# Kernel tuning notes

Measured on AMD Instinct MI355X. Metric: run time of the kernel, lower is better.

## Reference

```python
import jax, jax.numpy as jnp
import numpy as np

N = 262144  # points per batch (~4096 rays x 64 samples)
FDIM = 64   # plane feature dim
S = 512     # base plane resolution


def setup_inputs() -> dict:
    key = jax.random.key(0)
    ks = jax.random.split(key, 10)
    x = jax.random.uniform(ks[0], (N, 3), dtype=jnp.float32, minval=-1.0, maxval=1.0)
    rays_o = jnp.array([[0.0, 0.0, 1.5]], dtype=jnp.float32)  # ray origin; distances straddle 1.5/2.0
    scale = jnp.ones((3,), dtype=jnp.float32)
    plane = lambda k, s: jax.random.normal(k, (FDIM, s, s), dtype=jnp.float32)
    return {
        'x': x, 'rays_o': rays_o, 'scale': scale,
        'xy_plane': plane(ks[1], S), 'yz_plane': plane(ks[2], S), 'xz_plane': plane(ks[3], S),
        'xy_plane1': plane(ks[4], S // 2), 'yz_plane1': plane(ks[5], S // 2), 'xz_plane1': plane(ks[6], S // 2),
        'xy_plane2': plane(ks[7], S // 4), 'yz_plane2': plane(ks[8], S // 4), 'xz_plane2': plane(ks[9], S // 4),
    }


def bilinear_sample(plane, coords):
    """F.grid_sample(mode='bilinear', align_corners=True, padding_mode='zeros').
    plane: [C, H, W]; coords: [N, 2] with (x, y) in [-1, 1] (x indexes W).
    Returns [N, C]."""
    C, H, W = plane.shape
    fx = (coords[:, 0] + 1.0) * 0.5 * (W - 1)
    fy = (coords[:, 1] + 1.0) * 0.5 * (H - 1)
    x0 = jnp.floor(fx)
    y0 = jnp.floor(fy)
    wx = fx - x0
    wy = fy - y0
    x0i = x0.astype(jnp.int32)
    y0i = y0.astype(jnp.int32)

    def gather(xi, yi):
        valid = (xi >= 0) & (xi < W) & (yi >= 0) & (yi < H)
        xc = jnp.clip(xi, 0, W - 1)
        yc = jnp.clip(yi, 0, H - 1)
        v = plane[:, yc, xc]  # [C, N]
        return jnp.where(valid[None, :], v, 0.0)

    v00 = gather(x0i, y0i)
    v01 = gather(x0i + 1, y0i)
    v10 = gather(x0i, y0i + 1)
    v11 = gather(x0i + 1, y0i + 1)
    out = (v00 * (1 - wx) * (1 - wy) + v01 * wx * (1 - wy)
           + v10 * (1 - wx) * wy + v11 * wx * wy)  # [C, N]
    return out.T


def forward(x, rays_o, scale, xy0, yz0, xz0, xy1, yz1, xz1, xy2, yz2, xz2):
    xs = x * scale[None, :]
    xy_c = xs[:, :2]                                   # (x, y)
    xz_c = jnp.stack([xs[:, 0], xs[:, 2]], axis=-1)    # (x, z)
    yz_c = xs[:, 1:]                                   # (y, z)

    # laplace breakpoints: first index with distance > 1.5 / > 2.0 from rays_o[0]
    d = jnp.linalg.norm(rays_o[0][None, :] - xs, axis=-1)
    c1 = d > 1.5
    c2 = d > 2.0
    break1 = jnp.where(c1.any(), jnp.argmax(c1), 0)
    break2 = jnp.where(c2.any(), jnp.argmax(c2), 0)
    idx = jnp.arange(x.shape[0])
    # level 0: [0, break1), level 1: [break1, break2), level 2: [break2, N)
    level = jnp.where(idx < break1, 0, jnp.where(idx < break2, 1, 2))[:, None]

    def tri(p0, p1, p2, c):
        s0 = bilinear_sample(p0, c)
        s1 = bilinear_sample(p1, c)
        s2 = bilinear_sample(p2, c)
        # laplace: level1 = fine + half, level2 = fine + half + quarter
        return jnp.where(level == 0, s0, jnp.where(level == 1, s0 + s1, s0 + s1 + s2))

    return (tri(xy0, xy1, xy2, xy_c)
            + tri(xz0, xz1, xz2, xz_c)
            + tri(yz0, yz1, yz2, yz_c))


def reference(x, rays_o, scale, xy_plane, yz_plane, xz_plane, xy_plane1, yz_plane1, xz_plane1, xy_plane2, yz_plane2, xz_plane2):
    return forward(x, rays_o, scale, xy_plane, yz_plane, xz_plane,
                   xy_plane1, yz_plane1, xz_plane1,
                   xy_plane2, yz_plane2, xz_plane2)
```

## Files before the change

### kernel.cpp

```cpp
#include <hip/hip_runtime.h>
#include <hip/hip_fp16.h>

#define NPTS 262144
#define FDIM 64
#define NCELL 4096
#define NBLK 64
#define PPT 16

typedef float vfloat4 __attribute__((ext_vector_type(4)));

__global__ __launch_bounds__(256) void break_kernel(const float* __restrict__ x,
                                                    const float* __restrict__ rays_o,
                                                    const float* __restrict__ scale,
                                                    unsigned* __restrict__ breaks) {
  const unsigned t = blockIdx.x * 256u + threadIdx.x;
  const float r0 = rays_o[0], r1 = rays_o[1], r2 = rays_o[2];
  const float s0 = scale[0], s1 = scale[1], s2 = scale[2];
  unsigned b1 = 0xFFFFFFFFu, b2 = 0xFFFFFFFFu;
  for (unsigned p = t; p < NPTS; p += 65536u) {
    const float dx = r0 - x[p * 3 + 0] * s0;
    const float dy = r1 - x[p * 3 + 1] * s1;
    const float dz = r2 - x[p * 3 + 2] * s2;
    const float d = sqrtf(__fadd_rn(__fadd_rn(__fmul_rn(dx, dx), __fmul_rn(dy, dy)),
                                    __fmul_rn(dz, dz)));
    if (d > 1.5f) b1 = min(b1, p);
    if (d > 2.0f) b2 = min(b2, p);
  }
#pragma unroll
  for (int o = 32; o > 0; o >>= 1) {
    b1 = min(b1, (unsigned)__shfl_down((int)b1, o, 64));
    b2 = min(b2, (unsigned)__shfl_down((int)b2, o, 64));
  }
  if ((threadIdx.x & 63) == 0) {
    atomicMin(&breaks[0], b1);
    atomicMin(&breaks[1], b2);
  }
}

__device__ __forceinline__ unsigned part4(unsigned v) {
  v &= 15u;
  v = (v | (v << 4)) & 0x0C3u;
  v = (v | (v << 2)) & 0x249u;
  return v;
}

__device__ __forceinline__ unsigned cell_key(float x0, float x1, float x2) {
  const int cx = min(max((int)((x0 + 1.0f) * 8.0f), 0), 15);
  const int cy = min(max((int)((x1 + 1.0f) * 8.0f), 0), 15);
  const int cz = min(max((int)((x2 + 1.0f) * 8.0f), 0), 15);
  return part4((unsigned)cx) | (part4((unsigned)cy) << 1) | (part4((unsigned)cz) << 2);
}

__global__ __launch_bounds__(256) void bh_hist_kernel(const float* __restrict__ x,
                                                      const float* __restrict__ rays_o,
                                                      const float* __restrict__ scale,
                                                      unsigned* __restrict__ breaks,
                                                      unsigned short* __restrict__ keys,
                                                      unsigned* __restrict__ blockhist) {
  __shared__ unsigned lh[NCELL];
  for (int i = threadIdx.x; i < NCELL; i += 256) lh[i] = 0u;
  __syncthreads();
  const float r0 = rays_o[0], r1 = rays_o[1], r2 = rays_o[2];
  const float s0 = scale[0], s1 = scale[1], s2 = scale[2];
  const unsigned base = blockIdx.x * 256u + threadIdx.x;
  unsigned m1 = 0u, m2 = 0u;
#pragma unroll
  for (int k = 0; k < PPT; ++k) {
    const unsigned p = base + (unsigned)k * (NBLK * 256u);
    const float xs0 = x[p * 3 + 0] * s0;
    const float xs1 = x[p * 3 + 1] * s1;
    const float xs2 = x[p * 3 + 2] * s2;
    const float dx = r0 - xs0;
    const float dy = r1 - xs1;
    const float dz = r2 - xs2;
    const float d = sqrtf(__fadd_rn(__fadd_rn(__fmul_rn(dx, dx), __fmul_rn(dy, dy)),
                                    __fmul_rn(dz, dz)));
    if (d > 1.5f) m1 = max(m1, NPTS - p);
    if (d > 2.0f) m2 = max(m2, NPTS - p);
    const unsigned key = cell_key(xs0, xs1, xs2);
    atomicAdd(&lh[key], 1u);
    keys[p] = (unsigned short)key;
  }
#pragma unroll
  for (int o = 32; o > 0; o >>= 1) {
    m1 = max(m1, (unsigned)__shfl_down((int)m1, o, 64));
    m2 = max(m2, (unsigned)__shfl_down((int)m2, o, 64));
  }
  if ((threadIdx.x & 63) == 0) {
    atomicMax(&breaks[0], m1);
    atomicMax(&breaks[1], m2);
  }
  __syncthreads();
  unsigned* bh = blockhist + (size_t)blockIdx.x * NCELL;
  for (int i = threadIdx.x; i < NCELL; i += 256) bh[i] = lh[i];
}

__global__ __launch_bounds__(1024) void scan_kernel(unsigned* __restrict__ blockhist) {
  const int tid = threadIdx.x;
  uint4 acc = make_uint4(0u, 0u, 0u, 0u);
  for (int b = 0; b < NBLK; ++b) {
    const uint4 v = ((const uint4*)(blockhist + (size_t)b * NCELL))[tid];
    acc.x += v.x; acc.y += v.y; acc.z += v.z; acc.w += v.w;
  }
  const unsigned i0 = acc.x;
  const unsigned i1 = i0 + acc.y;
  const unsigned i2 = i1 + acc.z;
  const unsigned i3 = i2 + acc.w;
  __shared__ unsigned ls[1024];
  ls[tid] = i3;
  __syncthreads();
  for (int d = 1; d < 1024; d <<= 1) {
    const unsigned add = (tid >= d) ? ls[tid - d] : 0u;
    __syncthreads();
    ls[tid] += add;
    __syncthreads();
  }
  const unsigned base = ls[tid] - i3;
  uint4 run;
  run.x = base;
  run.y = base + i0;
  run.z = base + i1;
  run.w = base + i2;
  for (int b = 0; b < NBLK; ++b) {
    uint4* ptr = (uint4*)(blockhist + (size_t)b * NCELL) + tid;
    const uint4 v = *ptr;
    *ptr = run;
    run.x += v.x; run.y += v.y; run.z += v.z; run.w += v.w;
  }
}

__global__ __launch_bounds__(256) void scatter_kernel(const unsigned short* __restrict__ keys,
                                                      const unsigned* __restrict__ breaks,
                                                      const unsigned* __restrict__ blockhist,
                                                      unsigned* __restrict__ order) {
  __shared__ unsigned lh[NCELL];
  const unsigned* bh = blockhist + (size_t)blockIdx.x * NCELL;
  for (int i = threadIdx.x; i < NCELL; i += 256) lh[i] = bh[i];
  __syncthreads();
  unsigned b1 = NPTS - breaks[0]; if (b1 >= NPTS) b1 = 0u;
  unsigned b2 = NPTS - breaks[1]; if (b2 >= NPTS) b2 = 0u;
  const unsigned base = blockIdx.x * 256u + threadIdx.x;
#pragma unroll
  for (int k = 0; k < PPT; ++k) {
    const unsigned p = base + (unsigned)k * (NBLK * 256u);
    const unsigned key = keys[p];
    const unsigned pos = atomicAdd(&lh[key], 1u);
    const unsigned lvl = (p < b1) ? 0u : ((p < b2) ? 1u : 2u);
    order[pos] = p | (lvl << 18);
  }
}

#define TPIX 128

struct TransposeArgs {
  const float* src[9];
  __half* dst[9];
  int tile_hi[9];
  int SS[9];
};

union H8 { uint4 u; __half h[8]; };

__global__ __launch_bounds__(256) void transpose_all(TransposeArgs a) {
  const int tile = blockIdx.x;
  int pi = 0;
#pragma unroll
  for (int i = 0; i < 9; ++i) {
    if (tile >= a.tile_hi[i]) pi = i + 1;
  }
  const int lo = (pi == 0) ? 0 : a.tile_hi[pi - 1];
  const float* __restrict__ src = a.src[pi];
  __half* __restrict__ dst = a.dst[pi];
  const size_t SS = (size_t)a.SS[pi];

  const int ntm = (int)(SS / TPIX) - 1;
  const int tl = ((tile - lo) * 997) & ntm;

  const int t = threadIdx.x;
  const int slot = t >> 3;
  const int c8 = t & 7;
  const size_t p0 = (size_t)tl * TPIX + (size_t)slot * 4;
  const float* __restrict__ srcb = src + (size_t)(c8 * 8) * SS + p0;

  H8 h[4];
#pragma unroll
  for (int k = 0; k < 8; ++k) {
    const float4 v = *(const float4*)(srcb + (size_t)k * SS);
    h[0].h[k] = __float2half(v.x);
    h[1].h[k] = __float2half(v.y);
    h[2].h[k] = __float2half(v.z);
    h[3].h[k] = __float2half(v.w);
  }
#pragma unroll
  for (int r = 0; r < 4; ++r) {
    *(uint4*)(dst + (p0 + (size_t)r) * FDIM + c8 * 8) = h[r].u;
  }
}

__device__ __forceinline__ void bilinear_weights(int W, float cx, float cy,
                                                 float& w00, float& w01, float& w10, float& w11,
                                                 int& xc0, int& xc1, int& yc0, int& yc1) {
  const float Wm1 = (float)(W - 1);
  const float fx = (cx + 1.0f) * 0.5f * Wm1;
  const float fy = (cy + 1.0f) * 0.5f * Wm1;
  const float x0f = floorf(fx), y0f = floorf(fy);
  const float wx = fx - x0f, wy = fy - y0f;
  const int ix = (int)x0f, iy = (int)y0f;
  const int ix1 = ix + 1, iy1 = iy + 1;
  const bool vx0 = (ix >= 0) && (ix < W);
  const bool vx1 = (ix1 >= 0) && (ix1 < W);
  const bool vy0 = (iy >= 0) && (iy < W);
  const bool vy1 = (iy1 >= 0) && (iy1 < W);
  xc0 = min(max(ix, 0), W - 1);
  xc1 = min(max(ix1, 0), W - 1);
  yc0 = min(max(iy, 0), W - 1);
  yc1 = min(max(iy1, 0), W - 1);
  w00 = (1.0f - wx) * (1.0f - wy) * (float)(vx0 && vy0);
  w01 = wx * (1.0f - wy) * (float)(vx1 && vy0);
  w10 = (1.0f - wx) * wy * (float)(vx0 && vy1);
  w11 = wx * wy * (float)(vx1 && vy1);
}

__device__ __forceinline__ void sample8_t(const __half* __restrict__ pl, int W,
                                          float cx, float cy, int j8, float acc[8]) {
  float w00, w01, w10, w11;
  int xc0, xc1, yc0, yc1;
  bilinear_weights(W, cx, cy, w00, w01, w10, w11, xc0, xc1, yc0, yc1);
  const __half* b00 = pl + ((size_t)(yc0 * W + xc0) * FDIM + j8);
  const __half* b01 = pl + ((size_t)(yc0 * W + xc1) * FDIM + j8);
  const __half* b10 = pl + ((size_t)(yc1 * W + xc0) * FDIM + j8);
  const __half* b11 = pl + ((size_t)(yc1 * W + xc1) * FDIM + j8);
  H8 v00, v01, v10, v11;
  v00.u = *(const uint4*)b00;
  v01.u = *(const uint4*)b01;
  v10.u = *(const uint4*)b10;
  v11.u = *(const uint4*)b11;
#pragma unroll
  for (int k = 0; k < 8; ++k) {
    acc[k] += w00 * __half2float(v00.h[k]) + w01 * __half2float(v01.h[k]) +
              w10 * __half2float(v10.h[k]) + w11 * __half2float(v11.h[k]);
  }
}

__device__ __forceinline__ void sample8_d(const float* __restrict__ pl, int W,
                                          float cx, float cy, int j8, float acc[8]) {
  float w00, w01, w10, w11;
  int xc0, xc1, yc0, yc1;
  bilinear_weights(W, cx, cy, w00, w01, w10, w11, xc0, xc1, yc0, yc1);
  const size_t SS = (size_t)W * W;
  const int i00 = yc0 * W + xc0, i01 = yc0 * W + xc1;
  const int i10 = yc1 * W + xc0, i11 = yc1 * W + xc1;
#pragma unroll
  for (int k = 0; k < 8; ++k) {
    const size_t co = (size_t)(j8 + k) * SS;
    acc[k] += w00 * pl[co + i00] + w01 * pl[co + i01] +
              w10 * pl[co + i10] + w11 * pl[co + i11];
  }
}

struct PlanesH { const __half* p[9]; };
struct PlanesF { const float* p[9]; };

#define SAMPLE_BLOCKS (NPTS * 8 / 256)
#define XCD_CHUNK (SAMPLE_BLOCKS / 8)

__global__ __launch_bounds__(256) void sample_kernel(const float* __restrict__ x,
                                                     const float* __restrict__ scale,
                                                     const unsigned* __restrict__ order,
                                                     PlanesH tp, float* __restrict__ out) {
  const unsigned b = blockIdx.x;
  const unsigned sb = (b & 7u) * XCD_CHUNK + (b >> 3);
  const int t = (int)(sb * 256u + threadIdx.x);
  const int slot = t >> 3;
  const int j8 = (t & 7) * 8;
  const unsigned pk = order[slot];
  const int p = (int)(pk & 0x3FFFFu);
  const int level = (int)(pk >> 18);
  const float s0 = scale[0], s1 = scale[1], s2 = scale[2];
  const float xs0 = x[p * 3 + 0] * s0;
  const float xs1 = x[p * 3 + 1] * s1;
  const float xs2 = x[p * 3 + 2] * s2;
  float acc[8];
#pragma unroll
  for (int k = 0; k < 8; ++k) acc[k] = 0.0f;
  sample8_t(tp.p[0], 512, xs0, xs1, j8, acc);
  sample8_t(tp.p[1], 512, xs1, xs2, j8, acc);
  sample8_t(tp.p[2], 512, xs0, xs2, j8, acc);
  if (level >= 1) {
    sample8_t(tp.p[3], 256, xs0, xs1, j8, acc);
    sample8_t(tp.p[4], 256, xs1, xs2, j8, acc);
    sample8_t(tp.p[5], 256, xs0, xs2, j8, acc);
  }
  if (level >= 2) {
    sample8_t(tp.p[6], 128, xs0, xs1, j8, acc);
    sample8_t(tp.p[7], 128, xs1, xs2, j8, acc);
    sample8_t(tp.p[8], 128, xs0, xs2, j8, acc);
  }
  float* o = out + (size_t)p * FDIM + j8;
  vfloat4 lo = {acc[0], acc[1], acc[2], acc[3]};
  vfloat4 hi = {acc[4], acc[5], acc[6], acc[7]};
  __builtin_nontemporal_store(lo, (vfloat4*)o);
  __builtin_nontemporal_store(hi, (vfloat4*)(o + 4));
}

__global__ __launch_bounds__(256) void sample_kernel_direct(const float* __restrict__ x,
                                                            const float* __restrict__ scale,
                                                            const unsigned* __restrict__ breaks,
                                                            PlanesF tp, float* __restrict__ out) {
  const int t = blockIdx.x * 256 + threadIdx.x;
  const int p = t >> 3;
  const int j8 = (t & 7) * 8;
  const float s0 = scale[0], s1 = scale[1], s2 = scale[2];
  const float xs0 = x[p * 3 + 0] * s0;
  const float xs1 = x[p * 3 + 1] * s1;
  const float xs2 = x[p * 3 + 2] * s2;
  unsigned b1 = breaks[0]; if (b1 >= NPTS) b1 = 0;
  unsigned b2 = breaks[1]; if (b2 >= NPTS) b2 = 0;
  const unsigned pu = (unsigned)p;
  const int level = (pu < b1) ? 0 : ((pu < b2) ? 1 : 2);
  float acc[8];
#pragma unroll
  for (int k = 0; k < 8; ++k) acc[k] = 0.0f;
  sample8_d(tp.p[0], 512, xs0, xs1, j8, acc);
  sample8_d(tp.p[1], 512, xs1, xs2, j8, acc);
  sample8_d(tp.p[2], 512, xs0, xs2, j8, acc);
  if (level >= 1) {
    sample8_d(tp.p[3], 256, xs0, xs1, j8, acc);
    sample8_d(tp.p[4], 256, xs1, xs2, j8, acc);
    sample8_d(tp.p[5], 256, xs0, xs2, j8, acc);
  }
  if (level >= 2) {
    sample8_d(tp.p[6], 128, xs0, xs1, j8, acc);
    sample8_d(tp.p[7], 128, xs1, xs2, j8, acc);
    sample8_d(tp.p[8], 128, xs0, xs2, j8, acc);
  }
  float4* o4 = (float4*)(out + (size_t)p * FDIM + j8);
  o4[0] = make_float4(acc[0], acc[1], acc[2], acc[3]);
  o4[1] = make_float4(acc[4], acc[5], acc[6], acc[7]);
}

extern "C" void kernel_launch(void* const* d_in, const int* in_sizes, int n_in,
                              void* d_out, int out_size, void* d_ws, size_t ws_size,
                              hipStream_t stream) {
  const float* x = (const float*)d_in[0];
  const float* rays_o = (const float*)d_in[1];
  const float* scale = (const float*)d_in[2];
  const float* pl32[9];
  for (int i = 0; i < 9; ++i) pl32[i] = (const float*)d_in[3 + i];
  float* out = (float*)d_out;

  unsigned char* ws = (unsigned char*)d_ws;
  unsigned* breaks = (unsigned*)ws;
  unsigned short* keys = (unsigned short*)(ws + 256);
  unsigned* blockhist = (unsigned*)(ws + 256 + (size_t)NPTS * 2);
  unsigned* order = (unsigned*)(ws + 256 + (size_t)NPTS * 2 + (size_t)NBLK * NCELL * 4);
  const size_t planes_off = 256 + (size_t)NPTS * 2 + (size_t)NBLK * NCELL * 4 + (size_t)NPTS * 4;

  const int Ss[3] = {512, 256, 128};
  size_t need = planes_off;
  for (int l = 0; l < 3; ++l) need += 3 * (size_t)Ss[l] * Ss[l] * FDIM * sizeof(__half);

  if (ws_size >= need) {
    (void)hipMemsetAsync(d_ws, 0, 256, stream);

    bh_hist_kernel<<<NBLK, 256, 0, stream>>>(x, rays_o, scale, breaks, keys, blockhist);
    scan_kernel<<<1, 1024, 0, stream>>>(blockhist);
    scatter_kernel<<<NBLK, 256, 0, stream>>>(keys, breaks, blockhist, order);

    PlanesH tp;
    TransposeArgs ta;
    size_t off = planes_off;
    int tiles_acc = 0;
    for (int l = 0; l < 3; ++l) {
      const int S = Ss[l];
      const int SS = S * S;
      for (int o = 0; o < 3; ++o) {
        const int i = l * 3 + o;
        __half* dst = (__half*)(ws + off);
        tp.p[i] = dst;
        ta.src[i] = pl32[i];
        ta.dst[i] = dst;
        ta.SS[i] = SS;
        tiles_acc += SS / TPIX;
        ta.tile_hi[i] = tiles_acc;
        off += (size_t)SS * FDIM * sizeof(__half);
      }
    }
    transpose_all<<<tiles_acc, 256, 0, stream>>>(ta);
    sample_kernel<<<SAMPLE_BLOCKS, 256, 0, stream>>>(x, scale, order, tp, out);
  } else {
    (void)hipMemsetAsync(d_ws, 0xFF, 8, stream);
    break_kernel<<<256, 256, 0, stream>>>(x, rays_o, scale, breaks);
    PlanesF tf;
    for (int i = 0; i < 9; ++i) tf.p[i] = pl32[i];
    sample_kernel_direct<<<(NPTS * 8) / 256, 256, 0, stream>>>(x, scale, breaks, tf, out);
  }
}
```

Measured before the change: 426.4 us.

## Fuse histogram with plane transpose and fold scan into scatter kernel

The binning histogram kernel is merged with the plane transpose into one launch, with the first 64 blocks doing histogram work and the rest doing the transpose. The single-block scan kernel is removed, and each scatter block now recomputes its own prefix offsets by reading all block histograms. Transpose tiles grow to 1024 pixels, with each block looping over 8 sub-tiles. The aim is fewer launches and less serialization from the one-block scan, at the cost of redundant histogram reads in every scatter block and fewer, larger transpose blocks.

```diff
diff --git a/kernel.cpp b/kernel.cpp
--- a/kernel.cpp
+++ b/kernel.cpp
@@ -51,106 +51,8 @@
   return part4((unsigned)cx) | (part4((unsigned)cy) << 1) | (part4((unsigned)cz) << 2);
 }
 
-__global__ __launch_bounds__(256) void bh_hist_kernel(const float* __restrict__ x,
-                                                      const float* __restrict__ rays_o,
-                                                      const float* __restrict__ scale,
-                                                      unsigned* __restrict__ breaks,
-                                                      unsigned short* __restrict__ keys,
-                                                      unsigned* __restrict__ blockhist) {
-  __shared__ unsigned lh[NCELL];
-  for (int i = threadIdx.x; i < NCELL; i += 256) lh[i] = 0u;
-  __syncthreads();
-  const float r0 = rays_o[0], r1 = rays_o[1], r2 = rays_o[2];
-  const float s0 = scale[0], s1 = scale[1], s2 = scale[2];
-  const unsigned base = blockIdx.x * 256u + threadIdx.x;
-  unsigned m1 = 0u, m2 = 0u;
-#pragma unroll
-  for (int k = 0; k < PPT; ++k) {
-    const unsigned p = base + (unsigned)k * (NBLK * 256u);
-    const float xs0 = x[p * 3 + 0] * s0;
-    const float xs1 = x[p * 3 + 1] * s1;
-    const float xs2 = x[p * 3 + 2] * s2;
-    const float dx = r0 - xs0;
-    const float dy = r1 - xs1;
-    const float dz = r2 - xs2;
-    const float d = sqrtf(__fadd_rn(__fadd_rn(__fmul_rn(dx, dx), __fmul_rn(dy, dy)),
-                                    __fmul_rn(dz, dz)));
-    if (d > 1.5f) m1 = max(m1, NPTS - p);
-    if (d > 2.0f) m2 = max(m2, NPTS - p);
-    const unsigned key = cell_key(xs0, xs1, xs2);
-    atomicAdd(&lh[key], 1u);
-    keys[p] = (unsigned short)key;
-  }
-#pragma unroll
-  for (int o = 32; o > 0; o >>= 1) {
-    m1 = max(m1, (unsigned)__shfl_down((int)m1, o, 64));
-    m2 = max(m2, (unsigned)__shfl_down((int)m2, o, 64));
-  }
-  if ((threadIdx.x & 63) == 0) {
-    atomicMax(&breaks[0], m1);
-    atomicMax(&breaks[1], m2);
-  }
-  __syncthreads();
-  unsigned* bh = blockhist + (size_t)blockIdx.x * NCELL;
-  for (int i = threadIdx.x; i < NCELL; i += 256) bh[i] = lh[i];
-}
-
-__global__ __launch_bounds__(1024) void scan_kernel(unsigned* __restrict__ blockhist) {
-  const int tid = threadIdx.x;
-  uint4 acc = make_uint4(0u, 0u, 0u, 0u);
-  for (int b = 0; b < NBLK; ++b) {
-    const uint4 v = ((const uint4*)(blockhist + (size_t)b * NCELL))[tid];
-    acc.x += v.x; acc.y += v.y; acc.z += v.z; acc.w += v.w;
-  }
-  const unsigned i0 = acc.x;
-  const unsigned i1 = i0 + acc.y;
-  const unsigned i2 = i1 + acc.z;
-  const unsigned i3 = i2 + acc.w;
-  __shared__ unsigned ls[1024];
-  ls[tid] = i3;
-  __syncthreads();
-  for (int d = 1; d < 1024; d <<= 1) {
-    const unsigned add = (tid >= d) ? ls[tid - d] : 0u;
-    __syncthreads();
-    ls[tid] += add;
-    __syncthreads();
-  }
-  const unsigned base = ls[tid] - i3;
-  uint4 run;
-  run.x = base;
-  run.y = base + i0;
-  run.z = base + i1;
-  run.w = base + i2;
-  for (int b = 0; b < NBLK; ++b) {
-    uint4* ptr = (uint4*)(blockhist + (size_t)b * NCELL) + tid;
-    const uint4 v = *ptr;
-    *ptr = run;
-    run.x += v.x; run.y += v.y; run.z += v.z; run.w += v.w;
-  }
-}
-
-__global__ __launch_bounds__(256) void scatter_kernel(const unsigned short* __restrict__ keys,
-                                                      const unsigned* __restrict__ breaks,
-                                                      const unsigned* __restrict__ blockhist,
-                                                      unsigned* __restrict__ order) {
-  __shared__ unsigned lh[NCELL];
-  const unsigned* bh = blockhist + (size_t)blockIdx.x * NCELL;
-  for (int i = threadIdx.x; i < NCELL; i += 256) lh[i] = bh[i];
-  __syncthreads();
-  unsigned b1 = NPTS - breaks[0]; if (b1 >= NPTS) b1 = 0u;
-  unsigned b2 = NPTS - breaks[1]; if (b2 >= NPTS) b2 = 0u;
-  const unsigned base = blockIdx.x * 256u + threadIdx.x;
-#pragma unroll
-  for (int k = 0; k < PPT; ++k) {
-    const unsigned p = base + (unsigned)k * (NBLK * 256u);
-    const unsigned key = keys[p];
-    const unsigned pos = atomicAdd(&lh[key], 1u);
-    const unsigned lvl = (p < b1) ? 0u : ((p < b2) ? 1u : 2u);
-    order[pos] = p | (lvl << 18);
-  }
-}
-
-#define TPIX 128
+#define TPIX 1024
+#define SUBT 8
 
 struct TransposeArgs {
   const float* src[9];
@@ -161,8 +63,54 @@
 
 union H8 { uint4 u; __half h[8]; };
 
-__global__ __launch_bounds__(256) void transpose_all(TransposeArgs a) {
-  const int tile = blockIdx.x;
+__global__ __launch_bounds__(256) void fused_bh_transpose(const float* __restrict__ x,
+                                                          const float* __restrict__ rays_o,
+                                                          const float* __restrict__ scale,
+                                                          unsigned* __restrict__ breaks,
+                                                          unsigned short* __restrict__ keys,
+                                                          unsigned* __restrict__ blockhist,
+                                                          TransposeArgs a) {
+  __shared__ unsigned lh[NCELL];
+  const int bid = blockIdx.x;
+  if (bid < NBLK) {
+    for (int i = threadIdx.x; i < NCELL; i += 256) lh[i] = 0u;
+    __syncthreads();
+    const float r0 = rays_o[0], r1 = rays_o[1], r2 = rays_o[2];
+    const float s0 = scale[0], s1 = scale[1], s2 = scale[2];
+    const unsigned base = (unsigned)bid * 256u + threadIdx.x;
+    unsigned m1 = 0u, m2 = 0u;
+#pragma unroll
+    for (int k = 0; k < PPT; ++k) {
+      const unsigned p = base + (unsigned)k * (NBLK * 256u);
+      const float xs0 = x[p * 3 + 0] * s0;
+      const float xs1 = x[p * 3 + 1] * s1;
+      const float xs2 = x[p * 3 + 2] * s2;
+      const float dx = r0 - xs0;
+      const float dy = r1 - xs1;
+      const float dz = r2 - xs2;
+      const float d = sqrtf(__fadd_rn(__fadd_rn(__fmul_rn(dx, dx), __fmul_rn(dy, dy)),
+                                      __fmul_rn(dz, dz)));
+      if (d > 1.5f) m1 = max(m1, NPTS - p);
+      if (d > 2.0f) m2 = max(m2, NPTS - p);
+      const unsigned key = cell_key(xs0, xs1, xs2);
+      atomicAdd(&lh[key], 1u);
+      keys[p] = (unsigned short)key;
+    }
+#pragma unroll
+    for (int o = 32; o > 0; o >>= 1) {
+      m1 = max(m1, (unsigned)__shfl_down((int)m1, o, 64));
+      m2 = max(m2, (unsigned)__shfl_down((int)m2, o, 64));
+    }
+    if ((threadIdx.x & 63) == 0) {
+      atomicMax(&breaks[0], m1);
+      atomicMax(&breaks[1], m2);
+    }
+    __syncthreads();
+    unsigned* bh = blockhist + (size_t)bid * NCELL;
+    for (int i = threadIdx.x; i < NCELL; i += 256) bh[i] = lh[i];
+    return;
+  }
+  const int tile = bid - NBLK;
   int pi = 0;
 #pragma unroll
   for (int i = 0; i < 9; ++i) {
@@ -179,21 +127,93 @@
   const int t = threadIdx.x;
   const int slot = t >> 3;
   const int c8 = t & 7;
-  const size_t p0 = (size_t)tl * TPIX + (size_t)slot * 4;
-  const float* __restrict__ srcb = src + (size_t)(c8 * 8) * SS + p0;
-
-  H8 h[4];
-#pragma unroll
-  for (int k = 0; k < 8; ++k) {
-    const float4 v = *(const float4*)(srcb + (size_t)k * SS);
-    h[0].h[k] = __float2half(v.x);
-    h[1].h[k] = __float2half(v.y);
-    h[2].h[k] = __float2half(v.z);
-    h[3].h[k] = __float2half(v.w);
-  }
-#pragma unroll
-  for (int r = 0; r < 4; ++r) {
-    *(uint4*)(dst + (p0 + (size_t)r) * FDIM + c8 * 8) = h[r].u;
+  const size_t tb = (size_t)tl * TPIX;
+  const float* __restrict__ srcc = src + (size_t)(c8 * 8) * SS;
+
+#pragma unroll
+  for (int gi = 0; gi < SUBT; ++gi) {
+    const size_t p0 = tb + (size_t)gi * 128 + (size_t)slot * 4;
+    const float* __restrict__ srcb = srcc + p0;
+    H8 h[4];
+#pragma unroll
+    for (int k = 0; k < 8; ++k) {
+      const float4 v = *(const float4*)(srcb + (size_t)k * SS);
+      h[0].h[k] = __float2half(v.x);
+      h[1].h[k] = __float2half(v.y);
+      h[2].h[k] = __float2half(v.z);
+      h[3].h[k] = __float2half(v.w);
+    }
+#pragma unroll
+    for (int r = 0; r < 4; ++r) {
+      *(uint4*)(dst + (p0 + (size_t)r) * FDIM + c8 * 8) = h[r].u;
+    }
+  }
+}
+
+__global__ __launch_bounds__(256) void scatter_kernel(const unsigned short* __restrict__ keys,
+                                                      const unsigned* __restrict__ breaks,
+                                                      const unsigned* __restrict__ blockhist,
+                                                      unsigned* __restrict__ order) {
+  __shared__ unsigned base_lds[NCELL];
+  __shared__ unsigned ls[256];
+  const int tid = threadIdx.x;
+  const unsigned myb = blockIdx.x;
+
+  uint4 tot[4], par[4];
+#pragma unroll
+  for (int g = 0; g < 4; ++g) tot[g] = make_uint4(0u, 0u, 0u, 0u);
+#pragma unroll
+  for (int g = 0; g < 4; ++g) par[g] = make_uint4(0u, 0u, 0u, 0u);
+  for (unsigned bp = 0; bp < NBLK; ++bp) {
+    if (bp == myb) {
+#pragma unroll
+      for (int g = 0; g < 4; ++g) par[g] = tot[g];
+    }
+    const uint4* rp = (const uint4*)(blockhist + (size_t)bp * NCELL);
+#pragma unroll
+    for (int g = 0; g < 4; ++g) {
+      const uint4 v = rp[tid * 4 + g];
+      tot[g].x += v.x; tot[g].y += v.y; tot[g].z += v.z; tot[g].w += v.w;
+    }
+  }
+  unsigned tv[16], pv[16];
+#pragma unroll
+  for (int g = 0; g < 4; ++g) {
+    tv[g * 4 + 0] = tot[g].x; tv[g * 4 + 1] = tot[g].y;
+    tv[g * 4 + 2] = tot[g].z; tv[g * 4 + 3] = tot[g].w;
+    pv[g * 4 + 0] = par[g].x; pv[g * 4 + 1] = par[g].y;
+    pv[g * 4 + 2] = par[g].z; pv[g * 4 + 3] = par[g].w;
+  }
+  unsigned T = 0u;
+#pragma unroll
+  for (int j = 0; j < 16; ++j) T += tv[j];
+  ls[tid] = T;
+  __syncthreads();
+  for (int d = 1; d < 256; d <<= 1) {
+    const unsigned add = (tid >= d) ? ls[tid - d] : 0u;
+    __syncthreads();
+    ls[tid] += add;
+    __syncthreads();
+  }
+  unsigned running = ls[tid] - T;
+  const int c0 = tid * 16;
+#pragma unroll
+  for (int j = 0; j < 16; ++j) {
+    base_lds[c0 + j] = running + pv[j];
+    running += tv[j];
+  }
+  __syncthreads();
+
+  unsigned b1 = NPTS - breaks[0]; if (b1 >= NPTS) b1 = 0u;
+  unsigned b2 = NPTS - breaks[1]; if (b2 >= NPTS) b2 = 0u;
+  const unsigned base = myb * 256u + (unsigned)tid;
+#pragma unroll
+  for (int k = 0; k < PPT; ++k) {
+    const unsigned p = base + (unsigned)k * (NBLK * 256u);
+    const unsigned key = keys[p];
+    const unsigned pos = atomicAdd(&base_lds[key], 1u);
+    const unsigned lvl = (p < b1) ? 0u : ((p < b2) ? 1u : 2u);
+    order[pos] = p | (lvl << 18);
   }
 }
 
@@ -363,10 +383,6 @@
   if (ws_size >= need) {
     (void)hipMemsetAsync(d_ws, 0, 256, stream);
 
-    bh_hist_kernel<<<NBLK, 256, 0, stream>>>(x, rays_o, scale, breaks, keys, blockhist);
-    scan_kernel<<<1, 1024, 0, stream>>>(blockhist);
-    scatter_kernel<<<NBLK, 256, 0, stream>>>(keys, breaks, blockhist, order);
-
     PlanesH tp;
     TransposeArgs ta;
     size_t off = planes_off;
@@ -386,7 +402,9 @@
         off += (size_t)SS * FDIM * sizeof(__half);
       }
     }
-    transpose_all<<<tiles_acc, 256, 0, stream>>>(ta);
+    fused_bh_transpose<<<NBLK + tiles_acc, 256, 0, stream>>>(x, rays_o, scale,
+                                                             breaks, keys, blockhist, ta);
+    scatter_kernel<<<NBLK, 256, 0, stream>>>(keys, breaks, blockhist, order);
     sample_kernel<<<SAMPLE_BLOCKS, 256, 0, stream>>>(x, scale, order, tp, out);
   } else {
     (void)hipMemsetAsync(d_ws, 0xFF, 8, stream);
```

After: 413.3 us. 3.1% less time.

## Fuse histogram pass into plane transpose launch and parallelize the counting-sort scan

Applied to the files above, without the earlier changes.

The per-point cell histogram and break detection now share one launch with the fp32-to-fp16 plane transpose, so the small histogram work overlaps the bandwidth-bound transpose. Points are split into 256 contiguous chunks of 1024 instead of 64 strided blocks, which gives more parallel blocks. The single-block scan is replaced by a column scan across 16 blocks followed by a cell-total scan. The cost is a larger block histogram buffer and one extra small launch.

```diff
diff --git a/kernel.cpp b/kernel.cpp
--- a/kernel.cpp
+++ b/kernel.cpp
@@ -4,38 +4,11 @@
 #define NPTS 262144
 #define FDIM 64
 #define NCELL 4096
-#define NBLK 64
-#define PPT 16
+#define NCHUNK 256
+#define CPTS 1024
+#define BHPPT 4
 
 typedef float vfloat4 __attribute__((ext_vector_type(4)));
-
-__global__ __launch_bounds__(256) void break_kernel(const float* __restrict__ x,
-                                                    const float* __restrict__ rays_o,
-                                                    const float* __restrict__ scale,
-                                                    unsigned* __restrict__ breaks) {
-  const unsigned t = blockIdx.x * 256u + threadIdx.x;
-  const float r0 = rays_o[0], r1 = rays_o[1], r2 = rays_o[2];
-  const float s0 = scale[0], s1 = scale[1], s2 = scale[2];
-  unsigned b1 = 0xFFFFFFFFu, b2 = 0xFFFFFFFFu;
-  for (unsigned p = t; p < NPTS; p += 65536u) {
-    const float dx = r0 - x[p * 3 + 0] * s0;
-    const float dy = r1 - x[p * 3 + 1] * s1;
-    const float dz = r2 - x[p * 3 + 2] * s2;
-    const float d = sqrtf(__fadd_rn(__fadd_rn(__fmul_rn(dx, dx), __fmul_rn(dy, dy)),
-                                    __fmul_rn(dz, dz)));
-    if (d > 1.5f) b1 = min(b1, p);
-    if (d > 2.0f) b2 = min(b2, p);
-  }
-#pragma unroll
-  for (int o = 32; o > 0; o >>= 1) {
-    b1 = min(b1, (unsigned)__shfl_down((int)b1, o, 64));
-    b2 = min(b2, (unsigned)__shfl_down((int)b2, o, 64));
-  }
-  if ((threadIdx.x & 63) == 0) {
-    atomicMin(&breaks[0], b1);
-    atomicMin(&breaks[1], b2);
-  }
-}
 
 __device__ __forceinline__ unsigned part4(unsigned v) {
   v &= 15u;
@@ -51,61 +24,119 @@
   return part4((unsigned)cx) | (part4((unsigned)cy) << 1) | (part4((unsigned)cz) << 2);
 }
 
-__global__ __launch_bounds__(256) void bh_hist_kernel(const float* __restrict__ x,
-                                                      const float* __restrict__ rays_o,
-                                                      const float* __restrict__ scale,
-                                                      unsigned* __restrict__ breaks,
-                                                      unsigned short* __restrict__ keys,
-                                                      unsigned* __restrict__ blockhist) {
+#define TPIX 128
+
+struct TransposeArgs {
+  const float* src[9];
+  __half* dst[9];
+  int tile_hi[9];
+  int SS[9];
+};
+
+union H8 { uint4 u; __half h[8]; };
+
+__global__ __launch_bounds__(256) void fused_bh_transpose(const float* __restrict__ x,
+                                                          const float* __restrict__ rays_o,
+                                                          const float* __restrict__ scale,
+                                                          unsigned* __restrict__ breaks,
+                                                          unsigned short* __restrict__ keys,
+                                                          unsigned* __restrict__ blockhist,
+                                                          TransposeArgs a) {
   __shared__ unsigned lh[NCELL];
-  for (int i = threadIdx.x; i < NCELL; i += 256) lh[i] = 0u;
-  __syncthreads();
-  const float r0 = rays_o[0], r1 = rays_o[1], r2 = rays_o[2];
-  const float s0 = scale[0], s1 = scale[1], s2 = scale[2];
-  const unsigned base = blockIdx.x * 256u + threadIdx.x;
-  unsigned m1 = 0u, m2 = 0u;
-#pragma unroll
-  for (int k = 0; k < PPT; ++k) {
-    const unsigned p = base + (unsigned)k * (NBLK * 256u);
-    const float xs0 = x[p * 3 + 0] * s0;
-    const float xs1 = x[p * 3 + 1] * s1;
-    const float xs2 = x[p * 3 + 2] * s2;
-    const float dx = r0 - xs0;
-    const float dy = r1 - xs1;
-    const float dz = r2 - xs2;
-    const float d = sqrtf(__fadd_rn(__fadd_rn(__fmul_rn(dx, dx), __fmul_rn(dy, dy)),
-                                    __fmul_rn(dz, dz)));
-    if (d > 1.5f) m1 = max(m1, NPTS - p);
-    if (d > 2.0f) m2 = max(m2, NPTS - p);
-    const unsigned key = cell_key(xs0, xs1, xs2);
-    atomicAdd(&lh[key], 1u);
-    keys[p] = (unsigned short)key;
-  }
-#pragma unroll
-  for (int o = 32; o > 0; o >>= 1) {
-    m1 = max(m1, (unsigned)__shfl_down((int)m1, o, 64));
-    m2 = max(m2, (unsigned)__shfl_down((int)m2, o, 64));
-  }
-  if ((threadIdx.x & 63) == 0) {
-    atomicMax(&breaks[0], m1);
-    atomicMax(&breaks[1], m2);
-  }
-  __syncthreads();
-  unsigned* bh = blockhist + (size_t)blockIdx.x * NCELL;
-  for (int i = threadIdx.x; i < NCELL; i += 256) bh[i] = lh[i];
-}
-
-__global__ __launch_bounds__(1024) void scan_kernel(unsigned* __restrict__ blockhist) {
+  const int bid = blockIdx.x;
+  if (bid < NCHUNK) {
+    for (int i = threadIdx.x; i < NCELL; i += 256) lh[i] = 0u;
+    __syncthreads();
+    const float r0 = rays_o[0], r1 = rays_o[1], r2 = rays_o[2];
+    const float s0 = scale[0], s1 = scale[1], s2 = scale[2];
+    const unsigned pb = (unsigned)bid * (unsigned)CPTS + threadIdx.x;
+    unsigned m1 = 0u, m2 = 0u;
+#pragma unroll
+    for (int k = 0; k < BHPPT; ++k) {
+      const unsigned p = pb + (unsigned)k * 256u;
+      const float xs0 = x[p * 3 + 0] * s0;
+      const float xs1 = x[p * 3 + 1] * s1;
+      const float xs2 = x[p * 3 + 2] * s2;
+      const float dx = r0 - xs0;
+      const float dy = r1 - xs1;
+      const float dz = r2 - xs2;
+      const float d = sqrtf(__fadd_rn(__fadd_rn(__fmul_rn(dx, dx), __fmul_rn(dy, dy)),
+                                      __fmul_rn(dz, dz)));
+      if (d > 1.5f) m1 = max(m1, NPTS - p);
+      if (d > 2.0f) m2 = max(m2, NPTS - p);
+      const unsigned key = cell_key(xs0, xs1, xs2);
+      atomicAdd(&lh[key], 1u);
+      keys[p] = (unsigned short)key;
+    }
+#pragma unroll
+    for (int o = 32; o > 0; o >>= 1) {
+      m1 = max(m1, (unsigned)__shfl_down((int)m1, o, 64));
+      m2 = max(m2, (unsigned)__shfl_down((int)m2, o, 64));
+    }
+    if ((threadIdx.x & 63) == 0) {
+      atomicMax(&breaks[0], m1);
+      atomicMax(&breaks[1], m2);
+    }
+    __syncthreads();
+    unsigned* bh = blockhist + (size_t)bid * NCELL;
+    for (int i = threadIdx.x; i < NCELL; i += 256) bh[i] = lh[i];
+    return;
+  }
+  const int tile = bid - NCHUNK;
+  int pi = 0;
+#pragma unroll
+  for (int i = 0; i < 9; ++i) {
+    if (tile >= a.tile_hi[i]) pi = i + 1;
+  }
+  const int lo = (pi == 0) ? 0 : a.tile_hi[pi - 1];
+  const float* __restrict__ src = a.src[pi];
+  __half* __restrict__ dst = a.dst[pi];
+  const size_t SS = (size_t)a.SS[pi];
+
+  const int ntm = (int)(SS / TPIX) - 1;
+  const int tl = ((tile - lo) * 997) & ntm;
+
+  const int t = threadIdx.x;
+  const int slot = t >> 3;
+  const int c8 = t & 7;
+  const size_t p0 = (size_t)tl * TPIX + (size_t)slot * 4;
+  const float* __restrict__ srcb = src + (size_t)(c8 * 8) * SS + p0;
+
+  H8 h[4];
+#pragma unroll
+  for (int k = 0; k < 8; ++k) {
+    const float4 v = *(const float4*)(srcb + (size_t)k * SS);
+    h[0].h[k] = __float2half(v.x);
+    h[1].h[k] = __float2half(v.y);
+    h[2].h[k] = __float2half(v.z);
+    h[3].h[k] = __float2half(v.w);
+  }
+#pragma unroll
+  for (int r = 0; r < 4; ++r) {
+    *(uint4*)(dst + (p0 + (size_t)r) * FDIM + c8 * 8) = h[r].u;
+  }
+}
+
+__global__ __launch_bounds__(256) void scan_cols_kernel(unsigned* __restrict__ blockhist,
+                                                        unsigned* __restrict__ celltotal) {
+  const int c = blockIdx.x * 256 + threadIdx.x;
+  unsigned running = 0u;
+  for (int b = 0; b < NCHUNK; ++b) {
+    unsigned* p = blockhist + (size_t)b * NCELL + c;
+    const unsigned v = *p;
+    *p = running;
+    running += v;
+  }
+  celltotal[c] = running;
+}
+
+__global__ __launch_bounds__(1024) void scan_cells_kernel(unsigned* __restrict__ celltotal) {
   const int tid = threadIdx.x;
-  uint4 acc = make_uint4(0u, 0u, 0u, 0u);
-  for (int b = 0; b < NBLK; ++b) {
-    const uint4 v = ((const uint4*)(blockhist + (size_t)b * NCELL))[tid];
-    acc.x += v.x; acc.y += v.y; acc.z += v.z; acc.w += v.w;
-  }
-  const unsigned i0 = acc.x;
-  const unsigned i1 = i0 + acc.y;
-  const unsigned i2 = i1 + acc.z;
-  const unsigned i3 = i2 + acc.w;
+  uint4 h = ((uint4*)celltotal)[tid];
+  const unsigned i0 = h.x;
+  const unsigned i1 = i0 + h.y;
+  const unsigned i2 = i1 + h.z;
+  const unsigned i3 = i2 + h.w;
   __shared__ unsigned ls[1024];
   ls[tid] = i3;
   __syncthreads();
@@ -116,84 +147,34 @@
     __syncthreads();
   }
   const unsigned base = ls[tid] - i3;
-  uint4 run;
-  run.x = base;
-  run.y = base + i0;
-  run.z = base + i1;
-  run.w = base + i2;
-  for (int b = 0; b < NBLK; ++b) {
-    uint4* ptr = (uint4*)(blockhist + (size_t)b * NCELL) + tid;
-    const uint4 v = *ptr;
-    *ptr = run;
-    run.x += v.x; run.y += v.y; run.z += v.z; run.w += v.w;
-  }
+  uint4 o;
+  o.x = base;
+  o.y = base + i0;
+  o.z = base + i1;
+  o.w = base + i2;
+  ((uint4*)celltotal)[tid] = o;
 }
 
 __global__ __launch_bounds__(256) void scatter_kernel(const unsigned short* __restrict__ keys,
                                                       const unsigned* __restrict__ breaks,
                                                       const unsigned* __restrict__ blockhist,
+                                                      const unsigned* __restrict__ cellbase,
                                                       unsigned* __restrict__ order) {
   __shared__ unsigned lh[NCELL];
-  const unsigned* bh = blockhist + (size_t)blockIdx.x * NCELL;
-  for (int i = threadIdx.x; i < NCELL; i += 256) lh[i] = bh[i];
+  const unsigned u = blockIdx.x;
+  const unsigned* row = blockhist + (size_t)u * NCELL;
+  for (int i = threadIdx.x; i < NCELL; i += 256) lh[i] = row[i] + cellbase[i];
   __syncthreads();
   unsigned b1 = NPTS - breaks[0]; if (b1 >= NPTS) b1 = 0u;
   unsigned b2 = NPTS - breaks[1]; if (b2 >= NPTS) b2 = 0u;
-  const unsigned base = blockIdx.x * 256u + threadIdx.x;
-#pragma unroll
-  for (int k = 0; k < PPT; ++k) {
-    const unsigned p = base + (unsigned)k * (NBLK * 256u);
+  const unsigned pb = u * (unsigned)CPTS + threadIdx.x;
+#pragma unroll
+  for (int k = 0; k < BHPPT; ++k) {
+    const unsigned p = pb + (unsigned)k * 256u;
     const unsigned key = keys[p];
     const unsigned pos = atomicAdd(&lh[key], 1u);
     const unsigned lvl = (p < b1) ? 0u : ((p < b2) ? 1u : 2u);
     order[pos] = p | (lvl << 18);
-  }
-}
-
-#define TPIX 128
-
-struct TransposeArgs {
-  const float* src[9];
-  __half* dst[9];
-  int tile_hi[9];
-  int SS[9];
-};
-
-union H8 { uint4 u; __half h[8]; };
-
-__global__ __launch_bounds__(256) void transpose_all(TransposeArgs a) {
-  const int tile = blockIdx.x;
-  int pi = 0;
-#pragma unroll
-  for (int i = 0; i < 9; ++i) {
-    if (tile >= a.tile_hi[i]) pi = i + 1;
-  }
-  const int lo = (pi == 0) ? 0 : a.tile_hi[pi - 1];
-  const float* __restrict__ src = a.src[pi];
-  __half* __restrict__ dst = a.dst[pi];
-  const size_t SS = (size_t)a.SS[pi];
-
-  const int ntm = (int)(SS / TPIX) - 1;
-  const int tl = ((tile - lo) * 997) & ntm;
-
-  const int t = threadIdx.x;
-  const int slot = t >> 3;
-  const int c8 = t & 7;
-  const size_t p0 = (size_t)tl * TPIX + (size_t)slot * 4;
-  const float* __restrict__ srcb = src + (size_t)(c8 * 8) * SS + p0;
-
-  H8 h[4];
-#pragma unroll
-  for (int k = 0; k < 8; ++k) {
-    const float4 v = *(const float4*)(srcb + (size_t)k * SS);
-    h[0].h[k] = __float2half(v.x);
-    h[1].h[k] = __float2half(v.y);
-    h[2].h[k] = __float2half(v.z);
-    h[3].h[k] = __float2half(v.w);
-  }
-#pragma unroll
-  for (int r = 0; r < 4; ++r) {
-    *(uint4*)(dst + (p0 + (size_t)r) * FDIM + c8 * 8) = h[r].u;
   }
 }
 
@@ -303,6 +284,34 @@
   __builtin_nontemporal_store(hi, (vfloat4*)(o + 4));
 }
 
+__global__ __launch_bounds__(256) void break_kernel(const float* __restrict__ x,
+                                                    const float* __restrict__ rays_o,
+                                                    const float* __restrict__ scale,
+                                                    unsigned* __restrict__ breaks) {
+  const unsigned t = blockIdx.x * 256u + threadIdx.x;
+  const float r0 = rays_o[0], r1 = rays_o[1], r2 = rays_o[2];
+  const float s0 = scale[0], s1 = scale[1], s2 = scale[2];
+  unsigned b1 = 0xFFFFFFFFu, b2 = 0xFFFFFFFFu;
+  for (unsigned p = t; p < NPTS; p += 65536u) {
+    const float dx = r0 - x[p * 3 + 0] * s0;
+    const float dy = r1 - x[p * 3 + 1] * s1;
+    const float dz = r2 - x[p * 3 + 2] * s2;
+    const float d = sqrtf(__fadd_rn(__fadd_rn(__fmul_rn(dx, dx), __fmul_rn(dy, dy)),
+                                    __fmul_rn(dz, dz)));
+    if (d > 1.5f) b1 = min(b1, p);
+    if (d > 2.0f) b2 = min(b2, p);
+  }
+#pragma unroll
+  for (int o = 32; o > 0; o >>= 1) {
+    b1 = min(b1, (unsigned)__shfl_down((int)b1, o, 64));
+    b2 = min(b2, (unsigned)__shfl_down((int)b2, o, 64));
+  }
+  if ((threadIdx.x & 63) == 0) {
+    atomicMin(&breaks[0], b1);
+    atomicMin(&breaks[1], b2);
+  }
+}
+
 __global__ __launch_bounds__(256) void sample_kernel_direct(const float* __restrict__ x,
                                                             const float* __restrict__ scale,
                                                             const unsigned* __restrict__ breaks,
@@ -353,8 +362,11 @@
   unsigned* breaks = (unsigned*)ws;
   unsigned short* keys = (unsigned short*)(ws + 256);
   unsigned* blockhist = (unsigned*)(ws + 256 + (size_t)NPTS * 2);
-  unsigned* order = (unsigned*)(ws + 256 + (size_t)NPTS * 2 + (size_t)NBLK * NCELL * 4);
-  const size_t planes_off = 256 + (size_t)NPTS * 2 + (size_t)NBLK * NCELL * 4 + (size_t)NPTS * 4;
+  unsigned* celltotal = (unsigned*)(ws + 256 + (size_t)NPTS * 2 + (size_t)NCHUNK * NCELL * 4);
+  unsigned* order = (unsigned*)(ws + 256 + (size_t)NPTS * 2 + (size_t)NCHUNK * NCELL * 4 +
+                                (size_t)NCELL * 4);
+  const size_t planes_off = 256 + (size_t)NPTS * 2 + (size_t)NCHUNK * NCELL * 4 +
+                            (size_t)NCELL * 4 + (size_t)NPTS * 4;
 
   const int Ss[3] = {512, 256, 128};
   size_t need = planes_off;
@@ -362,10 +374,6 @@
 
   if (ws_size >= need) {
     (void)hipMemsetAsync(d_ws, 0, 256, stream);
-
-    bh_hist_kernel<<<NBLK, 256, 0, stream>>>(x, rays_o, scale, breaks, keys, blockhist);
-    scan_kernel<<<1, 1024, 0, stream>>>(blockhist);
-    scatter_kernel<<<NBLK, 256, 0, stream>>>(keys, breaks, blockhist, order);
 
     PlanesH tp;
     TransposeArgs ta;
@@ -386,13 +394,18 @@
         off += (size_t)SS * FDIM * sizeof(__half);
       }
     }
-    transpose_all<<<tiles_acc, 256, 0, stream>>>(ta);
+    fused_bh_transpose<<<NCHUNK + tiles_acc, 256, 0, stream>>>(x, rays_o, scale,
+                                                               breaks, keys, blockhist, ta);
+    scan_cols_kernel<<<NCELL / 256, 256, 0, stream>>>(blockhist, celltotal);
+    scan_cells_kernel<<<1, 1024, 0, stream>>>(celltotal);
+    scatter_kernel<<<NCHUNK, 256, 0, stream>>>(keys, breaks, blockhist, celltotal, order);
     sample_kernel<<<SAMPLE_BLOCKS, 256, 0, stream>>>(x, scale, order, tp, out);
   } else {
     (void)hipMemsetAsync(d_ws, 0xFF, 8, stream);
-    break_kernel<<<256, 256, 0, stream>>>(x, rays_o, scale, breaks);
+    break_kernel<<<256, 256, 0, stream>>>(x, rays_o, scale, (unsigned*)ws);
     PlanesF tf;
     for (int i = 0; i < 9; ++i) tf.p[i] = pl32[i];
-    sample_kernel_direct<<<(NPTS * 8) / 256, 256, 0, stream>>>(x, scale, breaks, tf, out);
-  }
-}
+    sample_kernel_direct<<<(NPTS * 8) / 256, 256, 0, stream>>>(x, scale, (unsigned*)ws,
+                                                               tf, out);
+  }
+}
```

Result: faster. 408.9 us (-4.1%).
